# Kernel optimization log

Measured on AMD Instinct MI355X. Metric: run time of the kernel, lower is better.

Reference implementation:

```python
import jax, jax.numpy as jnp
import numpy as np

IMG_C = 256
GC = 32  # graph_channel; must equal graph feature dim 32 for the residual


def setup_inputs() -> dict:
    key = jax.random.key(0)
    ks = jax.random.split(key, 10)
    B, N, WH_SIDE = 8, 4096, 64
    s = lambda fan_in: 1.0 / np.sqrt(fan_in)
    return {
        "input_graph": jax.random.normal(ks[0], (B, N, GC), jnp.float32),
        "input_image": jax.random.normal(ks[1], (B, IMG_C, WH_SIDE, WH_SIDE), jnp.float32),
        # Conv1d(kernel=1) weights stored as [out, in]
        "Wq": jax.random.uniform(ks[2], (GC, 32), jnp.float32, -s(32), s(32)),
        "bq": jax.random.uniform(ks[3], (GC,), jnp.float32, -s(32), s(32)),
        "Wk": jax.random.uniform(ks[4], (GC, IMG_C), jnp.float32, -s(IMG_C), s(IMG_C)),
        "bk": jax.random.uniform(ks[5], (GC,), jnp.float32, -s(IMG_C), s(IMG_C)),
        "Wv": jax.random.uniform(ks[6], (GC, IMG_C), jnp.float32, -s(IMG_C), s(IMG_C)),
        "bv": jax.random.uniform(ks[7], (GC,), jnp.float32, -s(IMG_C), s(IMG_C)),
        "Wc": jax.random.uniform(ks[8], (GC, GC), jnp.float32, -s(GC), s(GC)),
        "bc": jax.random.uniform(ks[9], (GC,), jnp.float32, -s(GC), s(GC)),
    }


def reference(input_graph, input_image, Wq, bq, Wk, bk, Wv, bv, Wc, bc):
    B, C, W, H = input_image.shape
    img = input_image.reshape(B, C, W * H)                      # [B, C, L]
    # 1x1 conv projections == channel matmuls
    K = jnp.einsum('oc,bcl->bol', Wk, img) + bk[None, :, None]  # [B, GC, L]
    V = jnp.einsum('oc,bcl->bol', Wv, img) + bv[None, :, None]  # [B, GC, L]
    # Q: graph [B, N, 32] -> conv over channel dim -> [B, N, GC]
    Q = jnp.einsum('oc,bnc->bno', Wq, input_graph) + bq[None, None, :]
    att = jnp.einsum('bno,bol->bnl', Q, K) / jnp.sqrt(jnp.float32(GC))  # [B, N, L]
    # NOTE: original softmax is over dim=1 (the node/query axis)
    att = jax.nn.softmax(att, axis=1)
    message = jnp.einsum('bol,bnl->bon', V, att)                # [B, GC, N]
    out = input_graph.transpose(0, 2, 1) + (
        jnp.einsum('oc,bcn->bon', Wc, message) + bc[None, :, None]
    )                                                           # [B, GC, N]
    return out.transpose(0, 2, 1)                               # [B, N, GC]
```

## Files before the change

### kernel.cpp

```cpp
#include <hip/hip_runtime.h>

#define BB 8
#define NN 4096
#define LL 4096
#define CC 256

typedef short bf16x8 __attribute__((ext_vector_type(8)));
typedef _Float16 f16x8 __attribute__((ext_vector_type(8)));
typedef __fp16 hf16x2 __attribute__((ext_vector_type(2)));
typedef float f32x4 __attribute__((ext_vector_type(4)));

__device__ __forceinline__ short f2bf(float f) {
  union { float f; unsigned u; } v; v.f = f;
  unsigned r = v.u + 0x7fffu + ((v.u >> 16) & 1u);
  return (short)(r >> 16);
}
__device__ __forceinline__ bf16x8 ld8(const float* __restrict__ fp) {
  float4 a = *(const float4*)fp;
  float4 b = *(const float4*)(fp + 4);
  bf16x8 r;
  r[0] = f2bf(a.x); r[1] = f2bf(a.y); r[2] = f2bf(a.z); r[3] = f2bf(a.w);
  r[4] = f2bf(b.x); r[5] = f2bf(b.y); r[6] = f2bf(b.z); r[7] = f2bf(b.w);
  return r;
}

__global__ __launch_bounds__(256) void ka_proj(
    const float* __restrict__ graph, const float* __restrict__ img,
    const float* __restrict__ Wq, const float* __restrict__ bq,
    const float* __restrict__ Wk, const float* __restrict__ bk,
    const float* __restrict__ Wv, const float* __restrict__ bv,
    short* __restrict__ Qb, short* __restrict__ Kt, _Float16* __restrict__ Vt,
    float* __restrict__ Zbuf)
{
  const int tid = threadIdx.x;
  const int w = tid >> 6, lane = tid & 63, lo = lane & 15, q = lane >> 4;
  const int bid = blockIdx.x;
  if (bid < 512) {
    const int b = bid >> 6;
    if (tid < 64) Zbuf[(size_t)b * LL + ((bid & 63) << 6) + tid] = 0.0f;
    const int lt = ((bid & 63) << 6) + (w << 4);
    f32x4 aK0 = {0,0,0,0}, aK1 = {0,0,0,0}, aV0 = {0,0,0,0}, aV1 = {0,0,0,0};
    const float* ib = img + (size_t)b * CC * LL + lt + lo;
    #pragma unroll
    for (int cs = 0; cs < 8; ++cs) {
      const int c0 = cs * 32 + q * 8;
      bf16x8 bi;
      #pragma unroll
      for (int j = 0; j < 8; ++j) bi[j] = f2bf(ib[(size_t)(c0 + j) * LL]);
      bf16x8 wk0 = ld8(Wk + lo * CC + c0);
      bf16x8 wk1 = ld8(Wk + (lo + 16) * CC + c0);
      bf16x8 wv0 = ld8(Wv + lo * CC + c0);
      bf16x8 wv1 = ld8(Wv + (lo + 16) * CC + c0);
      aK0 = __builtin_amdgcn_mfma_f32_16x16x32_bf16(wk0, bi, aK0, 0, 0, 0);
      aK1 = __builtin_amdgcn_mfma_f32_16x16x32_bf16(wk1, bi, aK1, 0, 0, 0);
      aV0 = __builtin_amdgcn_mfma_f32_16x16x32_bf16(wv0, bi, aV0, 0, 0, 0);
      aV1 = __builtin_amdgcn_mfma_f32_16x16x32_bf16(wv1, bi, aV1, 0, 0, 0);
    }
    const float kscale = 0.2550348663f;
    const size_t row = ((size_t)b * LL + lt + lo) * 32;
    short4 s0, s1;
    s0.x = f2bf((aK0[0] + bk[q * 4 + 0]) * kscale);
    s0.y = f2bf((aK0[1] + bk[q * 4 + 1]) * kscale);
    s0.z = f2bf((aK0[2] + bk[q * 4 + 2]) * kscale);
    s0.w = f2bf((aK0[3] + bk[q * 4 + 3]) * kscale);
    s1.x = f2bf((aK1[0] + bk[16 + q * 4 + 0]) * kscale);
    s1.y = f2bf((aK1[1] + bk[16 + q * 4 + 1]) * kscale);
    s1.z = f2bf((aK1[2] + bk[16 + q * 4 + 2]) * kscale);
    s1.w = f2bf((aK1[3] + bk[16 + q * 4 + 3]) * kscale);
    *(short4*)(Kt + row + q * 4) = s0;
    *(short4*)(Kt + row + 16 + q * 4) = s1;
    union { hf16x2 h[2]; uint2 u; } p0, p1;
    p0.h[0] = __builtin_amdgcn_cvt_pkrtz(aV0[0] + bv[q * 4 + 0], aV0[1] + bv[q * 4 + 1]);
    p0.h[1] = __builtin_amdgcn_cvt_pkrtz(aV0[2] + bv[q * 4 + 2], aV0[3] + bv[q * 4 + 3]);
    p1.h[0] = __builtin_amdgcn_cvt_pkrtz(aV1[0] + bv[16 + q * 4 + 0], aV1[1] + bv[16 + q * 4 + 1]);
    p1.h[1] = __builtin_amdgcn_cvt_pkrtz(aV1[2] + bv[16 + q * 4 + 2], aV1[3] + bv[16 + q * 4 + 3]);
    *(uint2*)(Vt + row + q * 4) = p0.u;
    *(uint2*)(Vt + row + 16 + q * 4) = p1.u;
  } else {
    const int t = bid - 512;
    const int b = t >> 6;
    const int nt = ((t & 63) << 6) + (w << 4);
    bf16x8 ag = ld8(graph + ((size_t)b * NN + nt + lo) * 32 + q * 8);
    bf16x8 w0 = ld8(Wq + lo * 32 + q * 8);
    bf16x8 w1 = ld8(Wq + (lo + 16) * 32 + q * 8);
    f32x4 z = {0,0,0,0};
    f32x4 a0 = __builtin_amdgcn_mfma_f32_16x16x32_bf16(ag, w0, z, 0, 0, 0);
    f32x4 a1 = __builtin_amdgcn_mfma_f32_16x16x32_bf16(ag, w1, z, 0, 0, 0);
    const float b0 = bq[lo], b1 = bq[lo + 16];
    #pragma unroll
    for (int r = 0; r < 4; ++r) {
      const size_t rowq = ((size_t)b * NN + nt + q * 4 + r) * 32;
      Qb[rowq + lo] = f2bf(a0[r] + b0);
      Qb[rowq + 16 + lo] = f2bf(a1[r] + b1);
    }
  }
}

__global__ __launch_bounds__(256) void kb1_z(
    const short* __restrict__ Qb, const short* __restrict__ Kt,
    float* __restrict__ Z)
{
  const int tid = threadIdx.x;
  const int w = tid >> 6, lane = tid & 63, lo = lane & 15, q = lane >> 4;
  const int bid = blockIdx.x;
  const int b = bid >> 8;
  const int l0 = ((bid >> 2) & 63) << 6;
  const int nq = bid & 3;
  bf16x8 kf[4];
  #pragma unroll
  for (int f = 0; f < 4; ++f)
    kf[f] = *(const bf16x8*)(Kt + ((size_t)b * LL + l0 + f * 16 + lo) * 32 + q * 8);
  float za[4][4] = {{0}};
  const short* qbase = Qb + ((size_t)b * NN + nq * 1024 + w * 256 + lo) * 32 + q * 8;
  #pragma unroll 4
  for (int it = 0; it < 16; ++it) {
    bf16x8 qf = *(const bf16x8*)(qbase + it * 512);
    #pragma unroll
    for (int f = 0; f < 4; ++f) {
      f32x4 z = {0,0,0,0};
      f32x4 c = __builtin_amdgcn_mfma_f32_16x16x32_bf16(kf[f], qf, z, 0, 0, 0);
      #pragma unroll
      for (int r = 0; r < 4; ++r) za[f][r] += __builtin_amdgcn_exp2f(c[r]);
    }
  }
  #pragma unroll
  for (int m = 1; m < 16; m <<= 1)
    #pragma unroll
    for (int f = 0; f < 4; ++f)
      #pragma unroll
      for (int r = 0; r < 4; ++r)
        za[f][r] += __shfl_xor(za[f][r], m, 64);
  if (lo == 0) {
    #pragma unroll
    for (int f = 0; f < 4; ++f)
      #pragma unroll
      for (int r = 0; r < 4; ++r)
        atomicAdd(&Z[(size_t)b * LL + l0 + f * 16 + q * 4 + r], za[f][r]);
  }
}

__global__ __launch_bounds__(256) void kb2_scale(
    const _Float16* __restrict__ Vt, const float* __restrict__ Z,
    _Float16* __restrict__ Vpp)
{
  const int tid = threadIdx.x;
  const int b = blockIdx.x >> 6;
  const int l = ((blockIdx.x & 63) << 6) + (tid & 63);
  const int og = tid >> 6;
  const float inv = __builtin_amdgcn_rcpf(Z[(size_t)b * LL + l]) * 4096.0f;
  const f16x8 vv = *(const f16x8*)(Vt + ((size_t)b * LL + l) * 32 + og * 8);
  #pragma unroll
  for (int j = 0; j < 8; ++j)
    Vpp[((size_t)b * 32 + og * 8 + j) * LL + l] = (_Float16)((float)vv[j] * inv);
}

__global__ __launch_bounds__(512, 4) void kc_attn(
    const short* __restrict__ Qb, const short* __restrict__ Kt,
    const _Float16* __restrict__ Vpp, const float* __restrict__ graph,
    const float* __restrict__ Wc, const float* __restrict__ bc,
    float* __restrict__ out)
{
  __shared__ __align__(16) unsigned char smem[8 * 32 * 72 * 2];
  const int tid = threadIdx.x;
  const int w = tid >> 6, lane = tid & 63, lo = lane & 15, q = lane >> 4;
  const int b = blockIdx.x >> 7;
  const int n0 = (blockIdx.x & 127) << 5;
  _Float16* Pw = (_Float16*)smem + w * (32 * 72);
  float* MS = (float*)smem;
  const bf16x8 qf0 = *(const bf16x8*)(Qb + ((size_t)b * NN + n0 + lo) * 32 + q * 8);
  const bf16x8 qf1 = *(const bf16x8*)(Qb + ((size_t)b * NN + n0 + 16 + lo) * 32 + q * 8);
  f32x4 m00 = {0,0,0,0}, m01 = {0,0,0,0}, m10 = {0,0,0,0}, m11 = {0,0,0,0};
  const short* ktb = Kt + (size_t)b * LL * 32 + lo * 32 + q * 8;
  const _Float16* vb0 = Vpp + ((size_t)b * 32 + lo) * LL;
  const _Float16* vb1 = vb0 + (size_t)16 * LL;
  const int lc0 = w * 8;
  bf16x8 kfN[4];
  #pragma unroll
  for (int f = 0; f < 4; ++f)
    kfN[f] = *(const bf16x8*)(ktb + (size_t)(lc0 * 64 + f * 16) * 32);
  for (int lc = lc0; lc < lc0 + 8; ++lc) {
    const int lbase = lc * 64;
    bf16x8 kfC[4];
    #pragma unroll
    for (int f = 0; f < 4; ++f) kfC[f] = kfN[f];
    f16x8 vA0 = *(const f16x8*)(vb0 + lbase + q * 8);
    f16x8 vA1 = *(const f16x8*)(vb0 + lbase + 32 + q * 8);
    f16x8 vB0 = *(const f16x8*)(vb1 + lbase + q * 8);
    f16x8 vB1 = *(const f16x8*)(vb1 + lbase + 32 + q * 8);
    const int lcn = (lc + 1 < lc0 + 8) ? lc + 1 : lc;
    #pragma unroll
    for (int f = 0; f < 4; ++f)
      kfN[f] = *(const bf16x8*)(ktb + (size_t)(lcn * 64 + f * 16) * 32);
    #pragma unroll
    for (int f = 0; f < 4; ++f) {
      f32x4 z = {0,0,0,0};
      f32x4 c0 = __builtin_amdgcn_mfma_f32_16x16x32_bf16(kfC[f], qf0, z, 0, 0, 0);
      f32x4 c1 = __builtin_amdgcn_mfma_f32_16x16x32_bf16(kfC[f], qf1, z, 0, 0, 0);
      union { hf16x2 h[2]; uint2 u; } pk0, pk1;
      pk0.h[0] = __builtin_amdgcn_cvt_pkrtz(__builtin_amdgcn_exp2f(c0[0]),
                                            __builtin_amdgcn_exp2f(c0[1]));
      pk0.h[1] = __builtin_amdgcn_cvt_pkrtz(__builtin_amdgcn_exp2f(c0[2]),
                                            __builtin_amdgcn_exp2f(c0[3]));
      pk1.h[0] = __builtin_amdgcn_cvt_pkrtz(__builtin_amdgcn_exp2f(c1[0]),
                                            __builtin_amdgcn_exp2f(c1[1]));
      pk1.h[1] = __builtin_amdgcn_cvt_pkrtz(__builtin_amdgcn_exp2f(c1[2]),
                                            __builtin_amdgcn_exp2f(c1[3]));
      *(uint2*)&Pw[lo * 72 + f * 16 + q * 4] = pk0.u;
      *(uint2*)&Pw[(16 + lo) * 72 + f * 16 + q * 4] = pk1.u;
    }
    {
      f16x8 pa00 = *(const f16x8*)&Pw[lo * 72 + q * 8];
      f16x8 pa01 = *(const f16x8*)&Pw[lo * 72 + 32 + q * 8];
      f16x8 pa10 = *(const f16x8*)&Pw[(16 + lo) * 72 + q * 8];
      f16x8 pa11 = *(const f16x8*)&Pw[(16 + lo) * 72 + 32 + q * 8];
      m00 = __builtin_amdgcn_mfma_f32_16x16x32_f16(pa00, vA0, m00, 0, 0, 0);
      m10 = __builtin_amdgcn_mfma_f32_16x16x32_f16(pa10, vA0, m10, 0, 0, 0);
      m01 = __builtin_amdgcn_mfma_f32_16x16x32_f16(pa00, vB0, m01, 0, 0, 0);
      m11 = __builtin_amdgcn_mfma_f32_16x16x32_f16(pa10, vB0, m11, 0, 0, 0);
      m00 = __builtin_amdgcn_mfma_f32_16x16x32_f16(pa01, vA1, m00, 0, 0, 0);
      m10 = __builtin_amdgcn_mfma_f32_16x16x32_f16(pa11, vA1, m10, 0, 0, 0);
      m01 = __builtin_amdgcn_mfma_f32_16x16x32_f16(pa01, vB1, m01, 0, 0, 0);
      m11 = __builtin_amdgcn_mfma_f32_16x16x32_f16(pa11, vB1, m11, 0, 0, 0);
    }
  }
  float* MSw = MS + w * (32 * 36);
  #pragma unroll
  for (int r = 0; r < 4; ++r) {
    MSw[(q * 4 + r) * 36 + lo] = m00[r];
    MSw[(q * 4 + r) * 36 + 16 + lo] = m01[r];
    MSw[(16 + q * 4 + r) * 36 + lo] = m10[r];
    MSw[(16 + q * 4 + r) * 36 + 16 + lo] = m11[r];
  }
  __syncthreads();
  if (tid < 288) {
    f32x4 s = *(const f32x4*)&MS[tid * 4];
    #pragma unroll
    for (int k = 1; k < 8; ++k) s += *(const f32x4*)&MS[k * 1152 + tid * 4];
    *(f32x4*)&MS[tid * 4] = s;
  }
  __syncthreads();
  const int o = lane & 31, nh = lane >> 5;
  const float bcv = bc[o];
  #pragma unroll
  for (int rr = 0; rr < 2; ++rr) {
    const int nl = w * 4 + nh * 2 + rr;
    f32x4 s = {0,0,0,0};
    #pragma unroll
    for (int cc = 0; cc < 8; ++cc) {
      f32x4 m4 = *(const f32x4*)&MS[nl * 36 + cc * 4];
      float4 wc4 = *(const float4*)(Wc + o * 32 + cc * 4);
      s[0] += wc4.x * m4[0];
      s[1] += wc4.y * m4[1];
      s[2] += wc4.z * m4[2];
      s[3] += wc4.w * m4[3];
    }
    const size_t idx = ((size_t)b * NN + n0 + nl) * 32 + o;
    out[idx] = (s[0] + s[1] + s[2] + s[3]) * (1.0f / 4096.0f) + bcv + graph[idx];
  }
}

extern "C" void kernel_launch(void* const* d_in, const int* in_sizes, int n_in,
                              void* d_out, int out_size, void* d_ws, size_t ws_size,
                              hipStream_t stream) {
  const float* graph = (const float*)d_in[0];
  const float* img   = (const float*)d_in[1];
  const float* Wq    = (const float*)d_in[2];
  const float* bq    = (const float*)d_in[3];
  const float* Wk    = (const float*)d_in[4];
  const float* bk    = (const float*)d_in[5];
  const float* Wv    = (const float*)d_in[6];
  const float* bv    = (const float*)d_in[7];
  const float* Wc    = (const float*)d_in[8];
  const float* bc    = (const float*)d_in[9];
  char* ws = (char*)d_ws;
  short*    Qb  = (short*)(ws + 0);
  short*    Kt  = (short*)(ws + 2097152);
  _Float16* Vt  = (_Float16*)(ws + 4194304);
  _Float16* Vpp = (_Float16*)(ws + 6291456);
  float*    Zb  = (float*)(ws + 8388608);
  ka_proj<<<dim3(1024), dim3(256), 0, stream>>>(graph, img, Wq, bq, Wk, bk, Wv, bv,
                                                Qb, Kt, Vt, Zb);
  kb1_z<<<dim3(2048), dim3(256), 0, stream>>>(Qb, Kt, Zb);
  kb2_scale<<<dim3(512), dim3(256), 0, stream>>>(Vt, Zb, Vpp);
  kc_attn<<<dim3(1024), dim3(512), 0, stream>>>(Qb, Kt, Vpp, graph, Wc, bc,
                                                (float*)d_out);
}
```

Measured before the change: 207.0 us.

## Restructure attention kernel to stage K/V tiles in shared memory with double buffering

The attention kernel now gives each block 128 nodes, with each wave owning 16 nodes, instead of splitting the L dimension across waves. K and V tiles are loaded cooperatively into double-buffered LDS, and the P·V step is software-pipelined one chunk behind the QK step. This removes the cross-wave reduction and cuts redundant global K/V reads, at the cost of a per-chunk __syncthreads and only 256 blocks. Block indexing in the Z kernel and the attention kernel is also interleaved by batch to spread the batches across the grid.

```diff
diff --git a/kernel.cpp b/kernel.cpp
--- a/kernel.cpp
+++ b/kernel.cpp
@@ -103,9 +103,10 @@
   const int tid = threadIdx.x;
   const int w = tid >> 6, lane = tid & 63, lo = lane & 15, q = lane >> 4;
   const int bid = blockIdx.x;
-  const int b = bid >> 8;
-  const int l0 = ((bid >> 2) & 63) << 6;
-  const int nq = bid & 3;
+  const int b = bid & 7;
+  const int t = bid >> 3;
+  const int l0 = (t & 63) << 6;
+  const int nq = t >> 6;
   bf16x8 kf[4];
   #pragma unroll
   for (int f = 0; f < 4; ++f)
@@ -154,107 +155,112 @@
     Vpp[((size_t)b * 32 + og * 8 + j) * LL + l] = (_Float16)((float)vv[j] * inv);
 }
 
-__global__ __launch_bounds__(512, 4) void kc_attn(
+#define KC2_BODY(LC, PW, PR, KC_, VC_, KN_, VN_, DOPV)                        \
+  {                                                                           \
+    const int lcn_ = ((LC) + 1 < 64) ? (LC) + 1 : (LC);                       \
+    uint2 kx_ = *(const uint2*)(kgsrc + (size_t)lcn_ * 2048);                 \
+    uint2 vx_ = *(const uint2*)(vgsrc + (size_t)lcn_ * 64);                   \
+    bf16x8 kf_[4];                                                            \
+    _Pragma("unroll")                                                         \
+    for (int f = 0; f < 4; ++f)                                               \
+      kf_[f] = *(const bf16x8*)((KC_) + (f * 16 + lo) * 40 + q * 8);          \
+    f16x8 nA0_ = *(const f16x8*)((VC_) + lo * 72 + q * 8);                    \
+    f16x8 nA1_ = *(const f16x8*)((VC_) + lo * 72 + 32 + q * 8);               \
+    f16x8 nB0_ = *(const f16x8*)((VC_) + (16 + lo) * 72 + q * 8);             \
+    f16x8 nB1_ = *(const f16x8*)((VC_) + (16 + lo) * 72 + 32 + q * 8);        \
+    if (DOPV) {                                                               \
+      f16x8 pa0_ = *(const f16x8*)((PR) + lo * 72 + q * 8);                   \
+      f16x8 pa1_ = *(const f16x8*)((PR) + lo * 72 + 32 + q * 8);              \
+      m00 = __builtin_amdgcn_mfma_f32_16x16x32_f16(pa0_, vA0, m00, 0, 0, 0);  \
+      m01 = __builtin_amdgcn_mfma_f32_16x16x32_f16(pa0_, vB0, m01, 0, 0, 0);  \
+      m00 = __builtin_amdgcn_mfma_f32_16x16x32_f16(pa1_, vA1, m00, 0, 0, 0);  \
+      m01 = __builtin_amdgcn_mfma_f32_16x16x32_f16(pa1_, vB1, m01, 0, 0, 0);  \
+    }                                                                         \
+    _Pragma("unroll")                                                         \
+    for (int f = 0; f < 4; ++f) {                                             \
+      f32x4 z_ = {0, 0, 0, 0};                                                \
+      f32x4 c_ = __builtin_amdgcn_mfma_f32_16x16x32_bf16(kf_[f], qf, z_, 0, 0, 0); \
+      union { hf16x2 h[2]; uint2 u; } pk_;                                    \
+      pk_.h[0] = __builtin_amdgcn_cvt_pkrtz(__builtin_amdgcn_exp2f(c_[0]),    \
+                                            __builtin_amdgcn_exp2f(c_[1]));   \
+      pk_.h[1] = __builtin_amdgcn_cvt_pkrtz(__builtin_amdgcn_exp2f(c_[2]),    \
+                                            __builtin_amdgcn_exp2f(c_[3]));   \
+      *(uint2*)&(PW)[lo * 72 + f * 16 + q * 4] = pk_.u;                       \
+    }                                                                         \
+    *(uint2*)((KN_) + kl * 40 + kc8 * 4) = kx_;                               \
+    *(uint2*)((VN_) + vo * 72 + vc16 * 4) = vx_;                              \
+    __syncthreads();                                                          \
+    vA0 = nA0_; vA1 = nA1_; vB0 = nB0_; vB1 = nB1_;                           \
+  }
+
+__global__ __launch_bounds__(512) void kc_attn(
     const short* __restrict__ Qb, const short* __restrict__ Kt,
     const _Float16* __restrict__ Vpp, const float* __restrict__ graph,
     const float* __restrict__ Wc, const float* __restrict__ bc,
     float* __restrict__ out)
 {
-  __shared__ __align__(16) unsigned char smem[8 * 32 * 72 * 2];
+  __shared__ __align__(16) unsigned char smem[56320];
   const int tid = threadIdx.x;
   const int w = tid >> 6, lane = tid & 63, lo = lane & 15, q = lane >> 4;
-  const int b = blockIdx.x >> 7;
-  const int n0 = (blockIdx.x & 127) << 5;
-  _Float16* Pw = (_Float16*)smem + w * (32 * 72);
-  float* MS = (float*)smem;
-  const bf16x8 qf0 = *(const bf16x8*)(Qb + ((size_t)b * NN + n0 + lo) * 32 + q * 8);
-  const bf16x8 qf1 = *(const bf16x8*)(Qb + ((size_t)b * NN + n0 + 16 + lo) * 32 + q * 8);
-  f32x4 m00 = {0,0,0,0}, m01 = {0,0,0,0}, m10 = {0,0,0,0}, m11 = {0,0,0,0};
-  const short* ktb = Kt + (size_t)b * LL * 32 + lo * 32 + q * 8;
-  const _Float16* vb0 = Vpp + ((size_t)b * 32 + lo) * LL;
-  const _Float16* vb1 = vb0 + (size_t)16 * LL;
-  const int lc0 = w * 8;
-  bf16x8 kfN[4];
-  #pragma unroll
-  for (int f = 0; f < 4; ++f)
-    kfN[f] = *(const bf16x8*)(ktb + (size_t)(lc0 * 64 + f * 16) * 32);
-  for (int lc = lc0; lc < lc0 + 8; ++lc) {
-    const int lbase = lc * 64;
-    bf16x8 kfC[4];
-    #pragma unroll
-    for (int f = 0; f < 4; ++f) kfC[f] = kfN[f];
-    f16x8 vA0 = *(const f16x8*)(vb0 + lbase + q * 8);
-    f16x8 vA1 = *(const f16x8*)(vb0 + lbase + 32 + q * 8);
-    f16x8 vB0 = *(const f16x8*)(vb1 + lbase + q * 8);
-    f16x8 vB1 = *(const f16x8*)(vb1 + lbase + 32 + q * 8);
-    const int lcn = (lc + 1 < lc0 + 8) ? lc + 1 : lc;
-    #pragma unroll
-    for (int f = 0; f < 4; ++f)
-      kfN[f] = *(const bf16x8*)(ktb + (size_t)(lcn * 64 + f * 16) * 32);
-    #pragma unroll
-    for (int f = 0; f < 4; ++f) {
-      f32x4 z = {0,0,0,0};
-      f32x4 c0 = __builtin_amdgcn_mfma_f32_16x16x32_bf16(kfC[f], qf0, z, 0, 0, 0);
-      f32x4 c1 = __builtin_amdgcn_mfma_f32_16x16x32_bf16(kfC[f], qf1, z, 0, 0, 0);
-      union { hf16x2 h[2]; uint2 u; } pk0, pk1;
-      pk0.h[0] = __builtin_amdgcn_cvt_pkrtz(__builtin_amdgcn_exp2f(c0[0]),
-                                            __builtin_amdgcn_exp2f(c0[1]));
-      pk0.h[1] = __builtin_amdgcn_cvt_pkrtz(__builtin_amdgcn_exp2f(c0[2]),
-                                            __builtin_amdgcn_exp2f(c0[3]));
-      pk1.h[0] = __builtin_amdgcn_cvt_pkrtz(__builtin_amdgcn_exp2f(c1[0]),
-                                            __builtin_amdgcn_exp2f(c1[1]));
-      pk1.h[1] = __builtin_amdgcn_cvt_pkrtz(__builtin_amdgcn_exp2f(c1[2]),
-                                            __builtin_amdgcn_exp2f(c1[3]));
-      *(uint2*)&Pw[lo * 72 + f * 16 + q * 4] = pk0.u;
-      *(uint2*)&Pw[(16 + lo) * 72 + f * 16 + q * 4] = pk1.u;
-    }
-    {
-      f16x8 pa00 = *(const f16x8*)&Pw[lo * 72 + q * 8];
-      f16x8 pa01 = *(const f16x8*)&Pw[lo * 72 + 32 + q * 8];
-      f16x8 pa10 = *(const f16x8*)&Pw[(16 + lo) * 72 + q * 8];
-      f16x8 pa11 = *(const f16x8*)&Pw[(16 + lo) * 72 + 32 + q * 8];
-      m00 = __builtin_amdgcn_mfma_f32_16x16x32_f16(pa00, vA0, m00, 0, 0, 0);
-      m10 = __builtin_amdgcn_mfma_f32_16x16x32_f16(pa10, vA0, m10, 0, 0, 0);
-      m01 = __builtin_amdgcn_mfma_f32_16x16x32_f16(pa00, vB0, m01, 0, 0, 0);
-      m11 = __builtin_amdgcn_mfma_f32_16x16x32_f16(pa10, vB0, m11, 0, 0, 0);
-      m00 = __builtin_amdgcn_mfma_f32_16x16x32_f16(pa01, vA1, m00, 0, 0, 0);
-      m10 = __builtin_amdgcn_mfma_f32_16x16x32_f16(pa11, vA1, m10, 0, 0, 0);
-      m01 = __builtin_amdgcn_mfma_f32_16x16x32_f16(pa01, vB1, m01, 0, 0, 0);
-      m11 = __builtin_amdgcn_mfma_f32_16x16x32_f16(pa11, vB1, m11, 0, 0, 0);
-    }
-  }
-  float* MSw = MS + w * (32 * 36);
+  const int b = blockIdx.x & 7;
+  const int n0 = ((int)blockIdx.x >> 3) << 7;
+  _Float16* PA = (_Float16*)smem + w * 2304;
+  _Float16* PB = PA + 1152;
+  short* KT0 = (short*)(smem + 36864);
+  short* KT1 = KT0 + 2560;
+  _Float16* VT0 = (_Float16*)(smem + 47104);
+  _Float16* VT1 = VT0 + 2304;
+  const bf16x8 qf = *(const bf16x8*)(Qb + ((size_t)b * NN + n0 + w * 16 + lo) * 32 + q * 8);
+  f32x4 m00 = {0,0,0,0}, m01 = {0,0,0,0};
+  const int kl = tid >> 3, kc8 = tid & 7;
+  const short* kgsrc = Kt + (size_t)b * LL * 32 + kl * 32 + kc8 * 4;
+  const int vo = tid >> 4, vc16 = tid & 15;
+  const _Float16* vgsrc = Vpp + ((size_t)b * 32 + vo) * LL + vc16 * 4;
+  {
+    uint2 kx = *(const uint2*)(kgsrc);
+    uint2 vx = *(const uint2*)(vgsrc);
+    *(uint2*)(KT0 + kl * 40 + kc8 * 4) = kx;
+    *(uint2*)(VT0 + vo * 72 + vc16 * 4) = vx;
+    __syncthreads();
+  }
+  f16x8 vA0 = {0,0,0,0,0,0,0,0}, vA1 = {0,0,0,0,0,0,0,0};
+  f16x8 vB0 = {0,0,0,0,0,0,0,0}, vB1 = {0,0,0,0,0,0,0,0};
+  #pragma unroll 1
+  for (int i2 = 0; i2 < 32; ++i2) {
+    const int lce = i2 * 2;
+    KC2_BODY(lce,     PA, PB, KT0, VT0, KT1, VT1, (i2 != 0));
+    KC2_BODY(lce + 1, PB, PA, KT1, VT1, KT0, VT0, true);
+  }
+  {
+    f16x8 pa0 = *(const f16x8*)(PB + lo * 72 + q * 8);
+    f16x8 pa1 = *(const f16x8*)(PB + lo * 72 + 32 + q * 8);
+    m00 = __builtin_amdgcn_mfma_f32_16x16x32_f16(pa0, vA0, m00, 0, 0, 0);
+    m01 = __builtin_amdgcn_mfma_f32_16x16x32_f16(pa0, vB0, m01, 0, 0, 0);
+    m00 = __builtin_amdgcn_mfma_f32_16x16x32_f16(pa1, vA1, m00, 0, 0, 0);
+    m01 = __builtin_amdgcn_mfma_f32_16x16x32_f16(pa1, vB1, m01, 0, 0, 0);
+  }
+  float* MSw = (float*)((unsigned char*)smem + w * 4608);
   #pragma unroll
   for (int r = 0; r < 4; ++r) {
     MSw[(q * 4 + r) * 36 + lo] = m00[r];
     MSw[(q * 4 + r) * 36 + 16 + lo] = m01[r];
-    MSw[(16 + q * 4 + r) * 36 + lo] = m10[r];
-    MSw[(16 + q * 4 + r) * 36 + 16 + lo] = m11[r];
-  }
-  __syncthreads();
-  if (tid < 288) {
-    f32x4 s = *(const f32x4*)&MS[tid * 4];
-    #pragma unroll
-    for (int k = 1; k < 8; ++k) s += *(const f32x4*)&MS[k * 1152 + tid * 4];
-    *(f32x4*)&MS[tid * 4] = s;
-  }
-  __syncthreads();
+  }
   const int o = lane & 31, nh = lane >> 5;
   const float bcv = bc[o];
   #pragma unroll
-  for (int rr = 0; rr < 2; ++rr) {
-    const int nl = w * 4 + nh * 2 + rr;
+  for (int rr = 0; rr < 8; ++rr) {
+    const int nl = nh * 8 + rr;
     f32x4 s = {0,0,0,0};
     #pragma unroll
     for (int cc = 0; cc < 8; ++cc) {
-      f32x4 m4 = *(const f32x4*)&MS[nl * 36 + cc * 4];
+      f32x4 m4 = *(const f32x4*)&MSw[nl * 36 + cc * 4];
       float4 wc4 = *(const float4*)(Wc + o * 32 + cc * 4);
       s[0] += wc4.x * m4[0];
       s[1] += wc4.y * m4[1];
       s[2] += wc4.z * m4[2];
       s[3] += wc4.w * m4[3];
     }
-    const size_t idx = ((size_t)b * NN + n0 + nl) * 32 + o;
+    const size_t idx = ((size_t)b * NN + n0 + w * 16 + nl) * 32 + o;
     out[idx] = (s[0] + s[1] + s[2] + s[3]) * (1.0f / 4096.0f) + bcv + graph[idx];
   }
 }
@@ -282,6 +288,6 @@
                                                 Qb, Kt, Vt, Zb);
   kb1_z<<<dim3(2048), dim3(256), 0, stream>>>(Qb, Kt, Zb);
   kb2_scale<<<dim3(512), dim3(256), 0, stream>>>(Vt, Zb, Vpp);
-  kc_attn<<<dim3(1024), dim3(512), 0, stream>>>(Qb, Kt, Vpp, graph, Wc, bc,
-                                                (float*)d_out);
-}
+  kc_attn<<<dim3(256), dim3(512), 0, stream>>>(Qb, Kt, Vpp, graph, Wc, bc,
+                                               (float*)d_out);
+}
```

Result: slower. 212.2 us (+2.5%).
